# Performance work log

Measured on AMD Instinct MI355X. Metric: run time of the kernel, lower is better.

The kernel has to match this reference:

```python
import jax, jax.numpy as jnp
import numpy as np

FS = 3          # filter_size
B, C, H, W = 16, 256, 96, 96
BN_EPS = 1e-5


def setup_inputs() -> dict:
    key = jax.random.key(0)
    ks = jax.random.split(key, 6)
    s = 0.05
    return {
        "x": jax.random.normal(ks[0], (B, C, H, W), jnp.float32),
        "convoluted": jax.random.normal(ks[1], (B, C, H, W), jnp.float32),
        # filter_gen_conv: 1x1 Conv2d(C -> C)
        "w_gen": jax.random.normal(ks[2], (C, C, 1, 1), jnp.float32) * s,
        "b_gen": jax.random.normal(ks[3], (C,), jnp.float32) * s,
        # c1: 3x3 Conv2d(C -> C) + BatchNorm2d(C) + ReLU
        "w_c1": jax.random.normal(ks[4], (C, C, 3, 3), jnp.float32) * s,
        "b_c1": jax.random.normal(ks[5], (C,), jnp.float32) * s,
        "gamma": jnp.ones((C,), jnp.float32),
        "beta": jnp.zeros((C,), jnp.float32),
    }


def reference(x, convoluted, w_gen, b_gen, w_c1, b_c1, gamma, beta):
    b, c, h, w = x.shape
    # adaptive_avg_pool2d(x, FS): H,W divisible by FS -> uniform bins
    pooled = x.reshape(b, c, FS, h // FS, FS, w // FS).mean(axis=(3, 5))  # [b,c,FS,FS]
    # 1x1 conv generating per-sample per-channel filters
    gen = jnp.einsum('bcij,oc->boij', pooled, w_gen[:, :, 0, 0]) + b_gen[None, :, None, None]

    # c1: conv3x3 (pad 1) + BatchNorm (training-mode batch stats) + ReLU
    y = jax.lax.conv_general_dilated(
        convoluted, w_c1, window_strides=(1, 1), padding=((1, 1), (1, 1)),
        dimension_numbers=('NCHW', 'OIHW', 'NCHW')) + b_c1[None, :, None, None]
    mu = y.mean(axis=(0, 2, 3), keepdims=True)
    var = y.var(axis=(0, 2, 3), keepdims=True)
    y = (y - mu) * jax.lax.rsqrt(var + BN_EPS)
    y = jax.nn.relu(y * gamma[None, :, None, None] + beta[None, :, None, None])

    # dynamic per-sample depthwise conv: groups = b*c, symmetric pad (FS odd)
    y = y.reshape(1, b * c, h, w)
    filt = gen.reshape(b * c, 1, FS, FS)
    pad = (FS - 1) // 2
    out = jax.lax.conv_general_dilated(
        y, filt, window_strides=(1, 1), padding=((pad, pad), (pad, pad)),
        feature_group_count=b * c, dimension_numbers=('NCHW', 'OIHW', 'NCHW'))
    return out.reshape(b, c, h, w)
```

## Files before the change

### kernel.cpp

```cpp
#include <hip/hip_runtime.h>

typedef __bf16 bf16x8 __attribute__((ext_vector_type(8)));
typedef float f32x4 __attribute__((ext_vector_type(4)));

static __device__ __forceinline__ ushort f2b(float f) {
    uint32_t x = __float_as_uint(f);
    x += 0x7fffu + ((x >> 16) & 1u);
    return (ushort)(x >> 16);
}
static __device__ __forceinline__ float b2f(ushort u) {
    return __uint_as_float(((uint32_t)u) << 16);
}

typedef const __attribute__((address_space(1))) uint32_t gu32;
typedef __attribute__((address_space(3))) uint32_t lu32;
static __device__ __forceinline__ void gl_lds16(const void* g, void* l) {
    __builtin_amdgcn_global_load_lds((gu32*)g, (lu32*)l, 16, 0, 0);
}

__global__ __launch_bounds__(256) void pool_k(const float* __restrict__ x,
                                              float* __restrict__ pooled) {
    const int bc  = blockIdx.x;
    const int tid = threadIdx.x;
    const int lane = tid & 63, wv = tid >> 6;
    const float4* p4 = (const float4*)(x + (size_t)bc * 9216);
    __shared__ float red[4][9];
#pragma unroll
    for (int bi = 0; bi < 3; ++bi) {
#pragma unroll
        for (int bj = 0; bj < 3; ++bj) {
            int row = bi * 32 + (tid >> 3);
            int c4  = bj * 8 + (tid & 7);
            float4 f = p4[row * 24 + c4];
            float s = f.x + f.y + f.z + f.w;
#pragma unroll
            for (int off = 32; off; off >>= 1) s += __shfl_down(s, off);
            if (lane == 0) red[wv][bi * 3 + bj] = s;
        }
    }
    __syncthreads();
    if (tid < 9) {
        float s = red[0][tid] + red[1][tid] + red[2][tid] + red[3][tid];
        pooled[(size_t)bc * 9 + tid] = s * (1.0f / 1024.0f);
    }
}

__global__ __launch_bounds__(256) void gen_k(const float* __restrict__ pooled,
                                             const float* __restrict__ wgen,
                                             const float* __restrict__ bgen,
                                             float* __restrict__ gen) {
    __shared__ float pl[256];
    const int b = blockIdx.x / 9, ij = blockIdx.x % 9;
    const int o = threadIdx.x;
    pl[o] = pooled[((size_t)b * 256 + o) * 9 + ij];
    __syncthreads();
    float a = bgen[o];
    const float4* wg4 = (const float4*)(wgen + (size_t)o * 256);
    const float4* pl4 = (const float4*)pl;
#pragma unroll 4
    for (int q = 0; q < 64; ++q) {
        float4 w = wg4[q], p = pl4[q];
        a += w.x * p.x + w.y * p.y + w.z * p.z + w.w * p.w;
    }
    gen[((size_t)b * 256 + o) * 9 + ij] = a;
}

__global__ __launch_bounds__(256) void wtr_k(const float* __restrict__ wc1,
                                             ushort* __restrict__ wtr) {
    int i = blockIdx.x * 256 + threadIdx.x;
    int tap = i >> 16;
    int rem = i & 65535;
    wtr[i] = f2b(wc1[(size_t)rem * 9 + tap]);
}

__global__ __launch_bounds__(512) void conv_k(const float* __restrict__ xin,
                                              const ushort* __restrict__ wtr,
                                              const float* __restrict__ bc1,
                                              ushort* __restrict__ yb) {
    __shared__ ushort Al[2][8192];
    __shared__ ushort Bl[15680];

    const int blk = blockIdx.x;
    const int b = blk / 48, hg = blk % 48, h0 = hg * 2;
    const int tid = threadIdx.x;
    const int lane = tid & 63, wv = tid >> 6;
    const int wm = wv & 3, wn = wv >> 2;
    const int lo = lane & 15, hi = lane >> 4;

    if (tid < 256) {
        int row = tid >> 6, pxp = ((tid >> 5) & 1) ? 97 : 0, c = tid & 31;
        Bl[(row * 98 + pxp) * 40 + c] = 0;
    }

    const int arow = wv * 32 + (lane >> 2);
    const int acc_ = (lane & 3) * 8;
    const int aoff0 = arow * 256 + acc_;
    const int aoff1 = aoff0 + 16 * 256;

    const float* gsrc[6];
    int loff[6];
    bool vld[6];
#pragma unroll
    for (int it = 0; it < 6; ++it) {
        int id = tid + it * 512;
        int c = id & 31, rq = id >> 5;
        int row = rq / 24, q = rq - row * 24;
        int r = h0 + row - 1;
        vld[it] = ((unsigned)r < 96u);
        int rs = vld[it] ? r : 0;
        gsrc[it] = xin + (size_t)b * 2359296 + (size_t)c * 9216 + rs * 96 + q * 4;
        loff[it] = (row * 98 + q * 4 + 1) * 40 + c;
    }

    f32x4 acc[4][6] = {};
    float4 f[6];

    gl_lds16(wtr + aoff0, &Al[0][wv * 1024]);
    gl_lds16(wtr + aoff1, &Al[0][wv * 1024 + 512]);
#pragma unroll
    for (int it = 0; it < 6; ++it) f[it] = *(const float4*)gsrc[it];
#pragma unroll
    for (int it = 0; it < 6; ++it) {
        ushort u0 = 0, u1 = 0, u2 = 0, u3 = 0;
        if (vld[it]) { u0 = f2b(f[it].x); u1 = f2b(f[it].y);
                       u2 = f2b(f[it].z); u3 = f2b(f[it].w); }
        ushort* wp = &Bl[loff[it]];
        wp[0] = u0; wp[40] = u1; wp[80] = u2; wp[120] = u3;
    }
    __syncthreads();

    int stp = 0;
    for (int ch = 0; ch < 8; ++ch) {
        if (ch < 7) {
#pragma unroll
            for (int it = 0; it < 6; ++it)
                f[it] = *(const float4*)(gsrc[it] + (size_t)(ch + 1) * 294912);
        }
#pragma unroll
        for (int tap = 0; tap < 9; ++tap, ++stp) {
            const int buf = stp & 1;
            if (stp < 71) {
                const int nst = stp + 1;
                const int ntap = nst % 9, nch = nst / 9;
                const ushort* as = wtr + ntap * 65536 + nch * 32;
                gl_lds16(as + aoff0, &Al[buf ^ 1][wv * 1024]);
                gl_lds16(as + aoff1, &Al[buf ^ 1][wv * 1024 + 512]);
            }
            const int dy = tap / 3, dx = tap % 3;
            bf16x8 af[4], bfr[6];
            const ushort* Ab = &Al[buf][0];
#pragma unroll
            for (int mi = 0; mi < 4; ++mi)
                af[mi] = *(const bf16x8*)(Ab + (wm * 64 + mi * 16 + lo) * 32 + hi * 8);
            const ushort* Bp = &Bl[((wn + dy) * 98 + lo + dx) * 40 + hi * 8];
#pragma unroll
            for (int ni = 0; ni < 6; ++ni)
                bfr[ni] = *(const bf16x8*)(Bp + ni * 640);
#pragma unroll
            for (int mi = 0; mi < 4; ++mi)
#pragma unroll
                for (int ni = 0; ni < 6; ++ni)
                    acc[mi][ni] = __builtin_amdgcn_mfma_f32_16x16x32_bf16(
                        af[mi], bfr[ni], acc[mi][ni], 0, 0, 0);
            if (tap == 8) {
                if (ch < 7) {
                    __syncthreads();
#pragma unroll
                    for (int it = 0; it < 6; ++it) {
                        ushort u0 = 0, u1 = 0, u2 = 0, u3 = 0;
                        if (vld[it]) { u0 = f2b(f[it].x); u1 = f2b(f[it].y);
                                       u2 = f2b(f[it].z); u3 = f2b(f[it].w); }
                        ushort* wp = &Bl[loff[it]];
                        wp[0] = u0; wp[40] = u1; wp[80] = u2; wp[120] = u3;
                    }
                    __syncthreads();
                }
            } else {
                __syncthreads();
            }
        }
    }

    const size_t ybase = (size_t)b * 2359296 + (size_t)(h0 + wn) * 96;
#pragma unroll
    for (int mi = 0; mi < 4; ++mi) {
        const int o0 = wm * 64 + mi * 16 + hi * 4;
#pragma unroll
        for (int rr = 0; rr < 4; ++rr) {
            const int o = o0 + rr;
            const float bias = bc1[o];
#pragma unroll
            for (int ni = 0; ni < 6; ++ni) {
                const int px = ni * 16 + lo;
                yb[ybase + (size_t)o * 9216 + px] = f2b(acc[mi][ni][rr] + bias);
            }
        }
    }
}

__global__ __launch_bounds__(256) void bnstat_k(const ushort* __restrict__ yb,
                                                float* __restrict__ part) {
    const int bc = blockIdx.x, tid = threadIdx.x;
    const ushort4* p4 = (const ushort4*)(yb + (size_t)bc * 9216);
    float s = 0.f, s2 = 0.f;
#pragma unroll
    for (int it = 0; it < 9; ++it) {
        ushort4 u = p4[tid + it * 256];
        float a = b2f(u.x), bb = b2f(u.y), c = b2f(u.z), d = b2f(u.w);
        s  += a + bb + c + d;
        s2 += a * a + bb * bb + c * c + d * d;
    }
    const int lane = tid & 63, wv = tid >> 6;
#pragma unroll
    for (int off = 32; off; off >>= 1) {
        s += __shfl_down(s, off);
        s2 += __shfl_down(s2, off);
    }
    __shared__ float r1[4], r2[4];
    if (lane == 0) { r1[wv] = s; r2[wv] = s2; }
    __syncthreads();
    if (tid == 0) part[bc]        = r1[0] + r1[1] + r1[2] + r1[3];
    if (tid == 1) part[4096 + bc] = r2[0] + r2[1] + r2[2] + r2[3];
}

__global__ __launch_bounds__(256) void bnfin_k(const float* __restrict__ part,
                                               const float* __restrict__ gamma,
                                               const float* __restrict__ beta,
                                               float* __restrict__ bnp) {
    const int c = threadIdx.x;
    float s = 0.f, s2 = 0.f;
#pragma unroll
    for (int b = 0; b < 16; ++b) {
        s  += part[b * 256 + c];
        s2 += part[4096 + b * 256 + c];
    }
    const float invN = 1.0f / 147456.0f;
    float mu  = s * invN;
    float var = s2 * invN - mu * mu;
    float sc  = gamma[c] * rsqrtf(var + 1e-5f);
    bnp[c]       = sc;
    bnp[256 + c] = beta[c] - mu * sc;
}

__global__ __launch_bounds__(256) void dw_k(const ushort* __restrict__ yb,
                                            const float* __restrict__ gen,
                                            const float* __restrict__ bnp,
                                            float* __restrict__ out) {
    __shared__ float pl[9216];
    const int bc = blockIdx.x, tid = threadIdx.x;
    const int c = bc & 255;
    const float sc = bnp[c], sh = bnp[256 + c];
    const ushort4* p4 = (const ushort4*)(yb + (size_t)bc * 9216);
#pragma unroll
    for (int it = 0; it < 9; ++it) {
        int v = tid + it * 256;
        ushort4 u = p4[v];
        float4 f;
        f.x = fmaxf(b2f(u.x) * sc + sh, 0.f);
        f.y = fmaxf(b2f(u.y) * sc + sh, 0.f);
        f.z = fmaxf(b2f(u.z) * sc + sh, 0.f);
        f.w = fmaxf(b2f(u.w) * sc + sh, 0.f);
        *(float4*)&pl[v * 4] = f;
    }
    float g[9];
    const float* gp = gen + (size_t)bc * 9;
#pragma unroll
    for (int k = 0; k < 9; ++k) g[k] = gp[k];
    __syncthreads();
    float* op = out + (size_t)bc * 9216;
#pragma unroll
    for (int it = 0; it < 36; ++it) {
        int i = tid + it * 256;
        int row = i / 96, col = i - row * 96;
        float a = 0.f;
#pragma unroll
        for (int dy = 0; dy < 3; ++dy) {
            int rr = row + dy - 1;
            if (rr < 0 || rr >= 96) continue;
#pragma unroll
            for (int dxq = 0; dxq < 3; ++dxq) {
                int cc = col + dxq - 1;
                if (cc < 0 || cc >= 96) continue;
                a += pl[rr * 96 + cc] * g[dy * 3 + dxq];
            }
        }
        op[i] = a;
    }
}

extern "C" void kernel_launch(void* const* d_in, const int* in_sizes, int n_in,
                              void* d_out, int out_size, void* d_ws, size_t ws_size,
                              hipStream_t stream) {
    const float* x       = (const float*)d_in[0];
    const float* conv_in = (const float*)d_in[1];
    const float* w_gen   = (const float*)d_in[2];
    const float* b_gen   = (const float*)d_in[3];
    const float* w_c1    = (const float*)d_in[4];
    const float* b_c1    = (const float*)d_in[5];
    const float* gamma   = (const float*)d_in[6];
    const float* beta    = (const float*)d_in[7];
    float* out = (float*)d_out;

    char* ws = (char*)d_ws;
    float*  pooled = (float*)(ws + 0);
    float*  gen    = (float*)(ws + 147456);
    ushort* wtr    = (ushort*)(ws + 294912);
    float*  part   = (float*)(ws + 1474560);
    float*  bnp    = (float*)(ws + 1507328);
    ushort* yb     = (ushort*)(ws + 1509376);

    pool_k  <<<4096, 256, 0, stream>>>(x, pooled);
    gen_k   <<<144,  256, 0, stream>>>(pooled, w_gen, b_gen, gen);
    wtr_k   <<<2304, 256, 0, stream>>>(w_c1, wtr);
    conv_k  <<<768,  512, 0, stream>>>(conv_in, wtr, b_c1, yb);
    bnstat_k<<<4096, 256, 0, stream>>>(yb, part);
    bnfin_k <<<1,    256, 0, stream>>>(part, gamma, beta, bnp);
    dw_k    <<<4096, 256, 0, stream>>>(yb, gen, bnp, out);
}
```

Before: 375.8 us.

## Pre-swizzle conv weights into per-step contiguous LDS layout

```diff
diff --git a/kernel.cpp b/kernel.cpp
--- a/kernel.cpp
+++ b/kernel.cpp
@@ -67,10 +67,17 @@
 
 __global__ __launch_bounds__(256) void wtr_k(const float* __restrict__ wc1,
                                              ushort* __restrict__ wtr) {
-    int i = blockIdx.x * 256 + threadIdx.x;
-    int tap = i >> 16;
-    int rem = i & 65535;
-    wtr[i] = f2b(wc1[(size_t)rem * 9 + tap]);
+    int g = blockIdx.x * 256 + threadIdx.x;
+    int step = g >> 10;
+    int hi   = (g >> 8) & 3;
+    int row  = g & 255;
+    int ch = step / 9, tap = step - ch * 9;
+    int cbase = ch * 32 + hi * 8;
+    ushort tmp[8];
+#pragma unroll
+    for (int j = 0; j < 8; ++j)
+        tmp[j] = f2b(wc1[(size_t)row * 2304 + (size_t)(cbase + j) * 9 + tap]);
+    *(uint4*)(wtr + (size_t)g * 8) = *(const uint4*)tmp;
 }
 
 __global__ __launch_bounds__(512) void conv_k(const float* __restrict__ xin,
@@ -92,10 +99,8 @@
         Bl[(row * 98 + pxp) * 40 + c] = 0;
     }
 
-    const int arow = wv * 32 + (lane >> 2);
-    const int acc_ = (lane & 3) * 8;
-    const int aoff0 = arow * 256 + acc_;
-    const int aoff1 = aoff0 + 16 * 256;
+    const int aoff0 = wv * 1024 + lane * 8;
+    const int aoff1 = aoff0 + 512;
 
     const float* gsrc[6];
     int loff[6];
@@ -112,6 +117,11 @@
         loff[it] = (row * 98 + q * 4 + 1) * 40 + c;
     }
 
+    int aro[4];
+#pragma unroll
+    for (int mi = 0; mi < 4; ++mi)
+        aro[mi] = hi * 2048 + (wm * 64 + mi * 16 + lo) * 8;
+
     f32x4 acc[4][6] = {};
     float4 f[6];
 
@@ -140,9 +150,7 @@
         for (int tap = 0; tap < 9; ++tap, ++stp) {
             const int buf = stp & 1;
             if (stp < 71) {
-                const int nst = stp + 1;
-                const int ntap = nst % 9, nch = nst / 9;
-                const ushort* as = wtr + ntap * 65536 + nch * 32;
+                const ushort* as = wtr + (size_t)(stp + 1) * 8192;
                 gl_lds16(as + aoff0, &Al[buf ^ 1][wv * 1024]);
                 gl_lds16(as + aoff1, &Al[buf ^ 1][wv * 1024 + 512]);
             }
@@ -151,7 +159,7 @@
             const ushort* Ab = &Al[buf][0];
 #pragma unroll
             for (int mi = 0; mi < 4; ++mi)
-                af[mi] = *(const bf16x8*)(Ab + (wm * 64 + mi * 16 + lo) * 32 + hi * 8);
+                af[mi] = *(const bf16x8*)(Ab + aro[mi]);
             const ushort* Bp = &Bl[((wn + dy) * 98 + lo + dx) * 40 + hi * 8];
 #pragma unroll
             for (int ni = 0; ni < 6; ++ni)
@@ -311,7 +319,7 @@
 
     pool_k  <<<4096, 256, 0, stream>>>(x, pooled);
     gen_k   <<<144,  256, 0, stream>>>(pooled, w_gen, b_gen, gen);
-    wtr_k   <<<2304, 256, 0, stream>>>(w_c1, wtr);
+    wtr_k   <<<288,  256, 0, stream>>>(w_c1, wtr);
     conv_k  <<<768,  512, 0, stream>>>(conv_in, wtr, b_c1, yb);
     bnstat_k<<<4096, 256, 0, stream>>>(yb, part);
     bnfin_k <<<1,    256, 0, stream>>>(part, gamma, beta, bnp);
```

Result: no change. 383.0 us (+1.9%).
